# Optimization experiments

Measured on AMD Instinct MI355X. Metric: run time of the kernel, lower is better.

The kernel has to match this reference:

```python
import jax, jax.numpy as jnp
import numpy as np

N = 50000
E = 600000
F_IN = 256
H = 128            # num_hidden_units * num_heads (heads=1)
C = 20             # num_classes
NEG_SLOPE = 0.2    # PyG GATConv default


def setup_inputs() -> dict:
    key = jax.random.key(0)
    ks = jax.random.split(key, 16)
    g = lambda k, shape, fan: jax.random.normal(k, shape, jnp.float32) / np.sqrt(fan)
    return {
        "x": jax.random.normal(ks[0], (N, F_IN), jnp.float32),
        "edge_index": jax.random.randint(ks[1], (2, E), 0, N, jnp.int64),
        # GATConv 1: F_IN -> H (heads=1, concat)
        "W1": g(ks[2], (F_IN, H), F_IN),
        "a_src1": g(ks[3], (H,), H),
        "a_dst1": g(ks[4], (H,), H),
        "b1": jnp.zeros((H,), jnp.float32),
        # GATConv 2: H -> H (heads=1)
        "W2": g(ks[5], (H, H), H),
        "a_src2": g(ks[6], (H,), H),
        "a_dst2": g(ks[7], (H,), H),
        "b2": jnp.zeros((H,), jnp.float32),
        # MLP head
        "Wm1": g(ks[8], (H, H), H),
        "bm1": jnp.zeros((H,), jnp.float32),
        "Wm2": g(ks[9], (H, C), H),
        "bm2": jnp.zeros((C,), jnp.float32),
    }


def gat_layer(x, W, a_src, a_dst, b, src, dst, n_nodes):
    """Single-head GATConv (PyG semantics, self-loops already in src/dst)."""
    h = x @ W                                    # [N, H]
    # edge attention logits: leaky_relu(a_src . h_j + a_dst . h_i)
    logits = jax.nn.leaky_relu((h @ a_src)[src] + (h @ a_dst)[dst], NEG_SLOPE)  # [Etot]
    # softmax over incoming edges per target node
    m = jax.ops.segment_max(logits, dst, num_segments=n_nodes)
    e = jnp.exp(logits - m[dst])
    denom = jax.ops.segment_sum(e, dst, num_segments=n_nodes)
    coef = e / denom[dst]                        # [Etot]
    out = jax.ops.segment_sum(coef[:, None] * h[src], dst, num_segments=n_nodes)
    return out + b


def reference(x, edge_index, W1, a_src1, a_dst1, b1, W2, a_src2, a_dst2, b2, Wm1, bm1, Wm2, bm2):
    n = x.shape[0]
    loops = jnp.arange(n, dtype=edge_index.dtype)
    src = jnp.concatenate([edge_index[0], loops])  # add self loops (GATConv default)
    dst = jnp.concatenate([edge_index[1], loops])
    h = gat_layer(x, W1, a_src1, a_dst1, b1, src, dst, n)
    h = jax.nn.relu(h)                            # dropout = identity at eval
    h = gat_layer(h, W2, a_src2, a_dst2, b2, src, dst, n)
    # MLP head: Linear -> (dropout) -> ReLU -> Linear -> sigmoid
    z = jax.nn.relu(h @ Wm1 + bm1)
    return jax.nn.sigmoid(z @ Wm2 + bm2)
```

## Files before the change

kernel.cpp:

```cpp
#include <hip/hip_runtime.h>
#include <math.h>

#define F_IN 256
#define HDIM 128
#define NCLS 20
#define NEG_SLOPE 0.2f
#define SCAN_CHUNK 1024

typedef float f32x4 __attribute__((ext_vector_type(4)));
typedef _Float16 f16x2 __attribute__((ext_vector_type(2)));
typedef _Float16 f16x4 __attribute__((ext_vector_type(4)));
typedef _Float16 f16x8 __attribute__((ext_vector_type(8)));

static __device__ __forceinline__ float lrelu(float x) { return x > 0.f ? x : NEG_SLOPE * x; }

__global__ void count_kernel(const int* __restrict__ ei, int E, int N, int* __restrict__ deg) {
    int e = blockIdx.x * blockDim.x + threadIdx.x;
    int Etot = E + N;
    if (e >= Etot) return;
    int d = (e < E) ? ei[E + e] : (e - E);
    atomicAdd(&deg[d], 1);
}

__global__ __launch_bounds__(256) void scan_reduce_kernel(const int* __restrict__ deg, int n,
                                                          int* __restrict__ bsums) {
    int base = blockIdx.x * SCAN_CHUNK + threadIdx.x * 4;
    int s = 0;
    if (base + 3 < n) {
        int4 v = *reinterpret_cast<const int4*>(&deg[base]);
        s = v.x + v.y + v.z + v.w;
    } else {
#pragma unroll
        for (int j = 0; j < 4; ++j) if (base + j < n) s += deg[base + j];
    }
#pragma unroll
    for (int o = 32; o > 0; o >>= 1) s += __shfl_down(s, o);
    __shared__ int ws[4];
    int lane = threadIdx.x & 63, w = threadIdx.x >> 6;
    if (lane == 0) ws[w] = s;
    __syncthreads();
    if (threadIdx.x == 0) bsums[blockIdx.x] = ws[0] + ws[1] + ws[2] + ws[3];
}

__global__ __launch_bounds__(256) void scan_bsums_kernel(int* __restrict__ bsums, int nb,
                                                         int* __restrict__ off, int n) {
    __shared__ int sh[256];
    int tid = threadIdx.x;
    int v = (tid < nb) ? bsums[tid] : 0;
    sh[tid] = v;
    __syncthreads();
    for (int d = 1; d < 256; d <<= 1) {
        int t = (tid >= d) ? sh[tid - d] : 0;
        __syncthreads();
        sh[tid] += t;
        __syncthreads();
    }
    if (tid < nb) bsums[tid] = sh[tid] - v;
    if (tid == 255) off[n] = sh[255];
}

__global__ __launch_bounds__(256) void scan_down_kernel(const int* __restrict__ deg, int n,
                                                        const int* __restrict__ bpre,
                                                        int* __restrict__ off) {
    int base = blockIdx.x * SCAN_CHUNK + threadIdx.x * 4;
    int v0 = 0, v1 = 0, v2 = 0, v3 = 0;
    if (base + 3 < n) {
        int4 t = *reinterpret_cast<const int4*>(&deg[base]);
        v0 = t.x; v1 = t.y; v2 = t.z; v3 = t.w;
    } else {
        if (base + 0 < n) v0 = deg[base + 0];
        if (base + 1 < n) v1 = deg[base + 1];
        if (base + 2 < n) v2 = deg[base + 2];
        if (base + 3 < n) v3 = deg[base + 3];
    }
    int tsum = v0 + v1 + v2 + v3;
    int lane = threadIdx.x & 63, w = threadIdx.x >> 6;
    int inc = tsum;
#pragma unroll
    for (int o = 1; o < 64; o <<= 1) {
        int t = __shfl_up(inc, o);
        if (lane >= o) inc += t;
    }
    int texc = inc - tsum;
    __shared__ int wsum[4];
    if (lane == 63) wsum[w] = inc;
    __syncthreads();
    int wpre = 0;
    for (int i = 0; i < w; ++i) wpre += wsum[i];
    int p = bpre[blockIdx.x] + wpre + texc;
    if (base + 3 < n) {
        int4 o4;
        o4.x = p; o4.y = p + v0; o4.z = p + v0 + v1; o4.w = p + v0 + v1 + v2;
        *reinterpret_cast<int4*>(&off[base]) = o4;
    } else {
        int run = p;
        if (base + 0 < n) { off[base + 0] = run; run += v0; }
        if (base + 1 < n) { off[base + 1] = run; run += v1; }
        if (base + 2 < n) { off[base + 2] = run; run += v2; }
        if (base + 3 < n) { off[base + 3] = run; }
    }
}

__global__ void scatter_kernel(const int* __restrict__ ei, int E, int N,
                               const int* __restrict__ off, int* __restrict__ cursor,
                               int* __restrict__ csr_src) {
    int e = blockIdx.x * blockDim.x + threadIdx.x;
    int Etot = E + N;
    if (e >= Etot) return;
    int s, d;
    if (e < E) { s = ei[e]; d = ei[E + e]; } else { s = d = e - E; }
    int pos = off[d] + atomicAdd(&cursor[d], 1);
    csr_src[pos] = s;
}

__global__ __launch_bounds__(64) void pack_b_kernel(const float* __restrict__ W1,
                                                    const float* __restrict__ W2,
                                                    const float* __restrict__ Wm1,
                                                    _Float16* __restrict__ p1,
                                                    _Float16* __restrict__ p2,
                                                    _Float16* __restrict__ p3) {
    int t = blockIdx.x;
    int lane = threadIdx.x;
    const float* B; _Float16* out; int r;
    if (t < 64)      { B = W1;  out = p1; r = t; }
    else if (t < 96) { B = W2;  out = p2; r = t - 64; }
    else             { B = Wm1; out = p3; r = t - 96; }
    int ks = r >> 3, cf = r & 7;
    int c  = cf * 16 + (lane & 15);
    int k0 = ks * 32 + (lane >> 4) * 8;
    size_t base = ((size_t)r * 64 + lane) * 16;
#pragma unroll
    for (int i = 0; i < 8; ++i) {
        float v = B[(size_t)(k0 + i) * 128 + c];
        _Float16 h = (_Float16)v;
        out[base + i]     = h;
        out[base + 8 + i] = (_Float16)(v - (float)h);
    }
}

template <int AFMT, int KSTEPS, int FUSE_HEAD>
__global__ __launch_bounds__(512) void gemm_mfma_kernel(
        const void* __restrict__ Aptr, const _Float16* __restrict__ Bp,
        _Float16* __restrict__ C, int M,
        const float* __restrict__ bias, int act,
        const float* __restrict__ a_src, const float* __restrict__ a_dst,
        float* __restrict__ as_out, float* __restrict__ ad_out,
        const float* __restrict__ Wh, const float* __restrict__ bh2,
        float* __restrict__ outp) {
    constexpr int K = KSTEPS * 32;
    __shared__ float sal[2][4][64];
    __shared__ float zs[FUSE_HEAD ? 64 : 1][FUSE_HEAD ? 132 : 1];
    __shared__ float Wt[FUSE_HEAD ? 20 : 1][FUSE_HEAD ? 132 : 1];
    __shared__ float bb[FUSE_HEAD ? 20 : 1];

    int tid = threadIdx.x;
    int lane = tid & 63;
    int wid = tid >> 6;
    int wr = wid >> 2, wc = wid & 3;
    int bm = blockIdx.x * 64;
    int l15 = lane & 15, l4 = lane >> 4;
    int row0 = bm + wr * 32 + l15;
    int koff = l4 * 8;

    if constexpr (FUSE_HEAD) {
        for (int i = tid; i < HDIM * NCLS; i += 512) Wt[i % NCLS][i / NCLS] = Wh[i];
        if (tid < NCLS) bb[tid] = bh2[tid];
    }

    const float*    A32 = (const float*)Aptr;
    const _Float16* A16 = (const _Float16*)Aptr;
    bool ok0 = row0 < M, ok1 = (row0 + 16) < M;
    const f16x8 zf = {0, 0, 0, 0, 0, 0, 0, 0};

    f32x4 acc[2][2];
#pragma unroll
    for (int m = 0; m < 2; ++m)
#pragma unroll
        for (int j = 0; j < 2; ++j) acc[m][j] = (f32x4){0.f, 0.f, 0.f, 0.f};

    auto loadA = [&](int ks, f16x8 a[2]) {
        int kb = ks * 32 + koff;
#pragma unroll
        for (int m = 0; m < 2; ++m) {
            int rr = row0 + m * 16;
            bool ok = m ? ok1 : ok0;
            if (AFMT == 0) {
                if (ok) {
                    const float* p = &A32[(size_t)rr * K + kb];
                    float4 u = *reinterpret_cast<const float4*>(p);
                    float4 w = *reinterpret_cast<const float4*>(p + 4);
                    f16x8 t;
                    t[0] = (_Float16)u.x; t[1] = (_Float16)u.y;
                    t[2] = (_Float16)u.z; t[3] = (_Float16)u.w;
                    t[4] = (_Float16)w.x; t[5] = (_Float16)w.y;
                    t[6] = (_Float16)w.z; t[7] = (_Float16)w.w;
                    a[m] = t;
                } else a[m] = zf;
            } else {
                a[m] = ok ? *reinterpret_cast<const f16x8*>(&A16[(size_t)rr * K + kb]) : zf;
            }
        }
    };
    auto loadB = [&](int ks, f16x8 bh[2], f16x8 bl[2]) {
#pragma unroll
        for (int j = 0; j < 2; ++j) {
            int cf = wc * 2 + j;
            const _Float16* p = Bp + (((size_t)ks * 8 + cf) * 64 + lane) * 16;
            bh[j] = *reinterpret_cast<const f16x8*>(p);
            bl[j] = *reinterpret_cast<const f16x8*>(p + 8);
        }
    };

    f16x8 a0[2], a1[2], bh0[2], bh1[2], bl0[2], bl1[2];
    loadA(0, a0); loadB(0, bh0, bl0);
#pragma unroll
    for (int ks = 0; ks < KSTEPS; ks += 2) {
        loadA(ks + 1, a1); loadB(ks + 1, bh1, bl1);
#pragma unroll
        for (int j = 0; j < 2; ++j) {
            acc[0][j] = __builtin_amdgcn_mfma_f32_16x16x32_f16(a0[0], bh0[j], acc[0][j], 0, 0, 0);
            acc[1][j] = __builtin_amdgcn_mfma_f32_16x16x32_f16(a0[1], bh0[j], acc[1][j], 0, 0, 0);
            acc[0][j] = __builtin_amdgcn_mfma_f32_16x16x32_f16(a0[0], bl0[j], acc[0][j], 0, 0, 0);
            acc[1][j] = __builtin_amdgcn_mfma_f32_16x16x32_f16(a0[1], bl0[j], acc[1][j], 0, 0, 0);
        }
        if (ks + 2 < KSTEPS) { loadA(ks + 2, a0); loadB(ks + 2, bh0, bl0); }
#pragma unroll
        for (int j = 0; j < 2; ++j) {
            acc[0][j] = __builtin_amdgcn_mfma_f32_16x16x32_f16(a1[0], bh1[j], acc[0][j], 0, 0, 0);
            acc[1][j] = __builtin_amdgcn_mfma_f32_16x16x32_f16(a1[1], bh1[j], acc[1][j], 0, 0, 0);
            acc[0][j] = __builtin_amdgcn_mfma_f32_16x16x32_f16(a1[0], bl1[j], acc[0][j], 0, 0, 0);
            acc[1][j] = __builtin_amdgcn_mfma_f32_16x16x32_f16(a1[1], bl1[j], acc[1][j], 0, 0, 0);
        }
    }

    float ps[2][4], pd[2][4];
#pragma unroll
    for (int m = 0; m < 2; ++m)
#pragma unroll
        for (int reg = 0; reg < 4; ++reg) { ps[m][reg] = 0.f; pd[m][reg] = 0.f; }

#pragma unroll
    for (int j = 0; j < 2; ++j) {
        int col = wc * 32 + j * 16 + l15;
        float bi = bias ? bias[col] : 0.f;
        float asc = a_src ? a_src[col] : 0.f;
        float adc = a_src ? a_dst[col] : 0.f;
#pragma unroll
        for (int m = 0; m < 2; ++m) {
#pragma unroll
            for (int reg = 0; reg < 4; ++reg) {
                int rloc = wr * 32 + m * 16 + l4 * 4 + reg;
                int rr = bm + rloc;
                float v = acc[m][j][reg] + bi;
                if (act) v = fmaxf(v, 0.f);
                if constexpr (FUSE_HEAD) {
                    zs[rloc][col] = v;
                } else {
                    if (rr < M) C[(size_t)rr * 128 + col] = (_Float16)v;
                }
                ps[m][reg] = fmaf(v, asc, ps[m][reg]);
                pd[m][reg] = fmaf(v, adc, pd[m][reg]);
            }
        }
    }

    if (a_src) {
#pragma unroll
        for (int o = 1; o < 16; o <<= 1) {
#pragma unroll
            for (int m = 0; m < 2; ++m)
#pragma unroll
                for (int reg = 0; reg < 4; ++reg) {
                    ps[m][reg] += __shfl_xor(ps[m][reg], o);
                    pd[m][reg] += __shfl_xor(pd[m][reg], o);
                }
        }
        if (l15 == 0) {
#pragma unroll
            for (int m = 0; m < 2; ++m)
#pragma unroll
                for (int reg = 0; reg < 4; ++reg) {
                    int rloc = wr * 32 + m * 16 + l4 * 4 + reg;
                    sal[0][wc][rloc] = ps[m][reg];
                    sal[1][wc][rloc] = pd[m][reg];
                }
        }
        __syncthreads();
        if (tid < 64) {
            int rr = bm + tid;
            if (rr < M) {
                as_out[rr] = sal[0][0][tid] + sal[0][1][tid] + sal[0][2][tid] + sal[0][3][tid];
                ad_out[rr] = sal[1][0][tid] + sal[1][1][tid] + sal[1][2][tid] + sal[1][3][tid];
            }
        }
    }

    if constexpr (FUSE_HEAD) {
        __syncthreads();
        for (int idx = tid; idx < 64 * NCLS; idx += 512) {
            int r = idx / NCLS, c = idx % NCLS;
            int rr = bm + r;
            if (rr >= M) continue;
            float s = bb[c];
#pragma unroll
            for (int k = 0; k < HDIM; k += 4) {
                float4 z4 = *reinterpret_cast<const float4*>(&zs[r][k]);
                float4 w4 = *reinterpret_cast<const float4*>(&Wt[c][k]);
                s = fmaf(z4.x, w4.x, s);
                s = fmaf(z4.y, w4.y, s);
                s = fmaf(z4.z, w4.z, s);
                s = fmaf(z4.w, w4.w, s);
            }
            outp[(size_t)rr * NCLS + c] = 1.f / (1.f + __expf(-s));
        }
    }
}

__global__ __launch_bounds__(256) void aggregate_kernel(const _Float16* __restrict__ h,
                                 const float* __restrict__ asrc, const float* __restrict__ adst,
                                 const int* __restrict__ off, const int* __restrict__ csr_src,
                                 const float* __restrict__ bias,
                                 _Float16* __restrict__ out,
                                 int N, int do_relu) {
    __shared__ float2 sm[4][64];
    int wslot = threadIdx.x >> 6;
    int wave = blockIdx.x * 4 + wslot;
    int lane = threadIdx.x & 63;
    if (wave >= N) return;
    int o0 = off[wave], o1 = off[wave + 1];
    float ad = adst[wave];
    int l31 = lane & 31;
    int jst = lane >> 5;

    float denom = 0.f;
    float4 aA = make_float4(0.f, 0.f, 0.f, 0.f);
    float4 aB = make_float4(0.f, 0.f, 0.f, 0.f);

    for (int base = o0; base < o1; base += 64) {
        int cnt = o1 - base; if (cnt > 64) cnt = 64;
        float e = 0.f; int s = 0;
        if (lane < cnt) {
            s = csr_src[base + lane];
            e = __expf(lrelu(asrc[s] + ad));
        }
        float t = e;
#pragma unroll
        for (int o = 32; o > 0; o >>= 1) t += __shfl_xor(t, o);
        denom += t;
        sm[wslot][lane] = make_float2(__int_as_float(s), e);

        int j = jst;
        for (; j + 2 < cnt; j += 4) {
            float2 s0 = sm[wslot][j];
            float2 s1 = sm[wslot][j + 2];
            f16x4 h0 = *reinterpret_cast<const f16x4*>(&h[(size_t)__float_as_int(s0.x) * HDIM + 4 * l31]);
            f16x4 h1 = *reinterpret_cast<const f16x4*>(&h[(size_t)__float_as_int(s1.x) * HDIM + 4 * l31]);
            aA.x = fmaf(s0.y, (float)h0[0], aA.x);
            aA.y = fmaf(s0.y, (float)h0[1], aA.y);
            aA.z = fmaf(s0.y, (float)h0[2], aA.z);
            aA.w = fmaf(s0.y, (float)h0[3], aA.w);
            aB.x = fmaf(s1.y, (float)h1[0], aB.x);
            aB.y = fmaf(s1.y, (float)h1[1], aB.y);
            aB.z = fmaf(s1.y, (float)h1[2], aB.z);
            aB.w = fmaf(s1.y, (float)h1[3], aB.w);
        }
        if (j < cnt) {
            float2 s0 = sm[wslot][j];
            f16x4 h0 = *reinterpret_cast<const f16x4*>(&h[(size_t)__float_as_int(s0.x) * HDIM + 4 * l31]);
            aA.x = fmaf(s0.y, (float)h0[0], aA.x);
            aA.y = fmaf(s0.y, (float)h0[1], aA.y);
            aA.z = fmaf(s0.y, (float)h0[2], aA.z);
            aA.w = fmaf(s0.y, (float)h0[3], aA.w);
        }
    }

    aA.x += aB.x; aA.y += aB.y; aA.z += aB.z; aA.w += aB.w;
    aA.x += __shfl_xor(aA.x, 32);
    aA.y += __shfl_xor(aA.y, 32);
    aA.z += __shfl_xor(aA.z, 32);
    aA.w += __shfl_xor(aA.w, 32);

    if (lane < 32) {
        float inv = 1.f / denom;
        float4 bi = *reinterpret_cast<const float4*>(&bias[4 * l31]);
        float v0 = aA.x * inv + bi.x;
        float v1 = aA.y * inv + bi.y;
        float v2 = aA.z * inv + bi.z;
        float v3 = aA.w * inv + bi.w;
        if (do_relu) {
            v0 = fmaxf(v0, 0.f); v1 = fmaxf(v1, 0.f);
            v2 = fmaxf(v2, 0.f); v3 = fmaxf(v3, 0.f);
        }
        f16x4 o4;
        o4[0] = (_Float16)v0; o4[1] = (_Float16)v1;
        o4[2] = (_Float16)v2; o4[3] = (_Float16)v3;
        *reinterpret_cast<f16x4*>(&out[(size_t)wave * HDIM + 4 * l31]) = o4;
    }
}

extern "C" void kernel_launch(void* const* d_in, const int* in_sizes, int n_in,
                              void* d_out, int out_size, void* d_ws, size_t ws_size,
                              hipStream_t stream) {
    const float* x      = (const float*)d_in[0];
    const int*   ei     = (const int*)d_in[1];
    const float* W1     = (const float*)d_in[2];
    const float* a_src1 = (const float*)d_in[3];
    const float* a_dst1 = (const float*)d_in[4];
    const float* b1     = (const float*)d_in[5];
    const float* W2     = (const float*)d_in[6];
    const float* a_src2 = (const float*)d_in[7];
    const float* a_dst2 = (const float*)d_in[8];
    const float* b2     = (const float*)d_in[9];
    const float* Wm1    = (const float*)d_in[10];
    const float* bm1    = (const float*)d_in[11];
    const float* Wm2    = (const float*)d_in[12];
    const float* bm2    = (const float*)d_in[13];

    int N = in_sizes[0] / F_IN;
    int E = in_sizes[1] / 2;
    int Etot = E + N;

    char* ws = (char*)d_ws;
    size_t pos = 0;
    auto alloc = [&](size_t bytes) -> void* {
        void* p = ws + pos;
        pos = (pos + bytes + 255) & ~(size_t)255;
        return p;
    };
    _Float16* h16 = (_Float16*)alloc((size_t)N * HDIM * 2);
    _Float16* f16 = (_Float16*)alloc((size_t)N * HDIM * 2);
    float* as_buf = (float*)alloc((size_t)N * 4);
    float* ad_buf = (float*)alloc((size_t)N * 4);
    int*   deg    = (int*)alloc((size_t)N * 4);
    int*   offs   = (int*)alloc((size_t)(N + 1) * 4);
    int*   cursor = (int*)alloc((size_t)N * 4);
    int*   csr    = (int*)alloc((size_t)Etot * 4);
    int*   bsums  = (int*)alloc(256 * 4);
    _Float16* p1 = (_Float16*)alloc(65536 * 2);
    _Float16* p2 = (_Float16*)alloc(32768 * 2);
    _Float16* p3 = (_Float16*)alloc(32768 * 2);

    hipMemsetAsync(deg, 0, (size_t)N * 4, stream);
    hipMemsetAsync(cursor, 0, (size_t)N * 4, stream);

    int eb = (Etot + 255) / 256;
    int nb = (N + SCAN_CHUNK - 1) / SCAN_CHUNK;
    count_kernel<<<eb, 256, 0, stream>>>(ei, E, N, deg);
    scan_reduce_kernel<<<nb, 256, 0, stream>>>(deg, N, bsums);
    scan_bsums_kernel<<<1, 256, 0, stream>>>(bsums, nb, offs, N);
    scan_down_kernel<<<nb, 256, 0, stream>>>(deg, N, bsums, offs);
    scatter_kernel<<<eb, 256, 0, stream>>>(ei, E, N, offs, cursor, csr);

    pack_b_kernel<<<128, 64, 0, stream>>>(W1, W2, Wm1, p1, p2, p3);

    int gemm_blocks = (N + 63) / 64;
    int wave_blocks = (N + 3) / 4;

    gemm_mfma_kernel<0, 8, 0><<<gemm_blocks, 512, 0, stream>>>(x, p1, h16, N, nullptr, 0,
                                                               a_src1, a_dst1, as_buf, ad_buf,
                                                               nullptr, nullptr, nullptr);
    aggregate_kernel<<<wave_blocks, 256, 0, stream>>>(h16, as_buf, ad_buf, offs, csr, b1, f16, N, 1);

    gemm_mfma_kernel<1, 4, 0><<<gemm_blocks, 512, 0, stream>>>(f16, p2, h16, N, nullptr, 0,
                                                               a_src2, a_dst2, as_buf, ad_buf,
                                                               nullptr, nullptr, nullptr);
    aggregate_kernel<<<wave_blocks, 256, 0, stream>>>(h16, as_buf, ad_buf, offs, csr, b2, f16, N, 0);

    gemm_mfma_kernel<1, 4, 1><<<gemm_blocks, 512, 0, stream>>>(f16, p3, h16, N, bm1, 1,
                                                               nullptr, nullptr, nullptr, nullptr,
                                                               Wm2, bm2, (float*)d_out);
}
```

Measured before the change: 227.3 us.

## Widen GEMM wave tiles to 4 column fragments and gather 8 halves per lane

The GEMM now runs 4 waves of 256 threads, each computing 32 rows by 64 columns. Each A fragment is reused across four B fragments, which halves redundant A loads and the cross-wave logit reduction, at the cost of more accumulator and B registers per wave. The aggregation kernel now has each lane gather 16-byte f16x8 chunks, so four edges are processed per wave iteration instead of two. That widens each memory request and moves more edges in flight, but replaces the two interleaved accumulators with a single strided loop and adds a two-step shuffle reduction.

```diff
diff --git a/kernel.cpp b/kernel.cpp
--- a/kernel.cpp
+++ b/kernel.cpp
@@ -139,7 +139,7 @@
 }
 
 template <int AFMT, int KSTEPS, int FUSE_HEAD>
-__global__ __launch_bounds__(512) void gemm_mfma_kernel(
+__global__ __launch_bounds__(256) void gemm_mfma_kernel(
         const void* __restrict__ Aptr, const _Float16* __restrict__ Bp,
         _Float16* __restrict__ C, int M,
         const float* __restrict__ bias, int act,
@@ -148,7 +148,7 @@
         const float* __restrict__ Wh, const float* __restrict__ bh2,
         float* __restrict__ outp) {
     constexpr int K = KSTEPS * 32;
-    __shared__ float sal[2][4][64];
+    __shared__ float sal[2][2][64];
     __shared__ float zs[FUSE_HEAD ? 64 : 1][FUSE_HEAD ? 132 : 1];
     __shared__ float Wt[FUSE_HEAD ? 20 : 1][FUSE_HEAD ? 132 : 1];
     __shared__ float bb[FUSE_HEAD ? 20 : 1];
@@ -156,14 +156,14 @@
     int tid = threadIdx.x;
     int lane = tid & 63;
     int wid = tid >> 6;
-    int wr = wid >> 2, wc = wid & 3;
+    int wr = wid >> 1, wc = wid & 1;
     int bm = blockIdx.x * 64;
     int l15 = lane & 15, l4 = lane >> 4;
     int row0 = bm + wr * 32 + l15;
     int koff = l4 * 8;
 
     if constexpr (FUSE_HEAD) {
-        for (int i = tid; i < HDIM * NCLS; i += 512) Wt[i % NCLS][i / NCLS] = Wh[i];
+        for (int i = tid; i < HDIM * NCLS; i += 256) Wt[i % NCLS][i / NCLS] = Wh[i];
         if (tid < NCLS) bb[tid] = bh2[tid];
     }
 
@@ -172,11 +172,11 @@
     bool ok0 = row0 < M, ok1 = (row0 + 16) < M;
     const f16x8 zf = {0, 0, 0, 0, 0, 0, 0, 0};
 
-    f32x4 acc[2][2];
+    f32x4 acc[2][4];
 #pragma unroll
     for (int m = 0; m < 2; ++m)
 #pragma unroll
-        for (int j = 0; j < 2; ++j) acc[m][j] = (f32x4){0.f, 0.f, 0.f, 0.f};
+        for (int j = 0; j < 4; ++j) acc[m][j] = (f32x4){0.f, 0.f, 0.f, 0.f};
 
     auto loadA = [&](int ks, f16x8 a[2]) {
         int kb = ks * 32 + koff;
@@ -201,23 +201,23 @@
             }
         }
     };
-    auto loadB = [&](int ks, f16x8 bh[2], f16x8 bl[2]) {
-#pragma unroll
-        for (int j = 0; j < 2; ++j) {
-            int cf = wc * 2 + j;
+    auto loadB = [&](int ks, f16x8 bh[4], f16x8 bl[4]) {
+#pragma unroll
+        for (int j = 0; j < 4; ++j) {
+            int cf = wc * 4 + j;
             const _Float16* p = Bp + (((size_t)ks * 8 + cf) * 64 + lane) * 16;
             bh[j] = *reinterpret_cast<const f16x8*>(p);
             bl[j] = *reinterpret_cast<const f16x8*>(p + 8);
         }
     };
 
-    f16x8 a0[2], a1[2], bh0[2], bh1[2], bl0[2], bl1[2];
+    f16x8 a0[2], a1[2], bh0[4], bh1[4], bl0[4], bl1[4];
     loadA(0, a0); loadB(0, bh0, bl0);
 #pragma unroll
     for (int ks = 0; ks < KSTEPS; ks += 2) {
         loadA(ks + 1, a1); loadB(ks + 1, bh1, bl1);
 #pragma unroll
-        for (int j = 0; j < 2; ++j) {
+        for (int j = 0; j < 4; ++j) {
             acc[0][j] = __builtin_amdgcn_mfma_f32_16x16x32_f16(a0[0], bh0[j], acc[0][j], 0, 0, 0);
             acc[1][j] = __builtin_amdgcn_mfma_f32_16x16x32_f16(a0[1], bh0[j], acc[1][j], 0, 0, 0);
             acc[0][j] = __builtin_amdgcn_mfma_f32_16x16x32_f16(a0[0], bl0[j], acc[0][j], 0, 0, 0);
@@ -225,7 +225,7 @@
         }
         if (ks + 2 < KSTEPS) { loadA(ks + 2, a0); loadB(ks + 2, bh0, bl0); }
 #pragma unroll
-        for (int j = 0; j < 2; ++j) {
+        for (int j = 0; j < 4; ++j) {
             acc[0][j] = __builtin_amdgcn_mfma_f32_16x16x32_f16(a1[0], bh1[j], acc[0][j], 0, 0, 0);
             acc[1][j] = __builtin_amdgcn_mfma_f32_16x16x32_f16(a1[1], bh1[j], acc[1][j], 0, 0, 0);
             acc[0][j] = __builtin_amdgcn_mfma_f32_16x16x32_f16(a1[0], bl1[j], acc[0][j], 0, 0, 0);
@@ -240,8 +240,8 @@
         for (int reg = 0; reg < 4; ++reg) { ps[m][reg] = 0.f; pd[m][reg] = 0.f; }
 
 #pragma unroll
-    for (int j = 0; j < 2; ++j) {
-        int col = wc * 32 + j * 16 + l15;
+    for (int j = 0; j < 4; ++j) {
+        int col = wc * 64 + j * 16 + l15;
         float bi = bias ? bias[col] : 0.f;
         float asc = a_src ? a_src[col] : 0.f;
         float adc = a_src ? a_dst[col] : 0.f;
@@ -289,15 +289,15 @@
         if (tid < 64) {
             int rr = bm + tid;
             if (rr < M) {
-                as_out[rr] = sal[0][0][tid] + sal[0][1][tid] + sal[0][2][tid] + sal[0][3][tid];
-                ad_out[rr] = sal[1][0][tid] + sal[1][1][tid] + sal[1][2][tid] + sal[1][3][tid];
+                as_out[rr] = sal[0][0][tid] + sal[0][1][tid];
+                ad_out[rr] = sal[1][0][tid] + sal[1][1][tid];
             }
         }
     }
 
     if constexpr (FUSE_HEAD) {
         __syncthreads();
-        for (int idx = tid; idx < 64 * NCLS; idx += 512) {
+        for (int idx = tid; idx < 64 * NCLS; idx += 256) {
             int r = idx / NCLS, c = idx % NCLS;
             int rr = bm + r;
             if (rr >= M) continue;
@@ -329,12 +329,13 @@
     if (wave >= N) return;
     int o0 = off[wave], o1 = off[wave + 1];
     float ad = adst[wave];
-    int l31 = lane & 31;
-    int jst = lane >> 5;
+    int l15 = lane & 15;
+    int eslot = lane >> 4;
 
     float denom = 0.f;
-    float4 aA = make_float4(0.f, 0.f, 0.f, 0.f);
-    float4 aB = make_float4(0.f, 0.f, 0.f, 0.f);
+    float acc[8];
+#pragma unroll
+    for (int i = 0; i < 8; ++i) acc[i] = 0.f;
 
     for (int base = o0; base < o1; base += 64) {
         int cnt = o1 - base; if (cnt > 64) cnt = 64;
@@ -348,53 +349,34 @@
         for (int o = 32; o > 0; o >>= 1) t += __shfl_xor(t, o);
         denom += t;
         sm[wslot][lane] = make_float2(__int_as_float(s), e);
-
-        int j = jst;
-        for (; j + 2 < cnt; j += 4) {
-            float2 s0 = sm[wslot][j];
-            float2 s1 = sm[wslot][j + 2];
-            f16x4 h0 = *reinterpret_cast<const f16x4*>(&h[(size_t)__float_as_int(s0.x) * HDIM + 4 * l31]);
-            f16x4 h1 = *reinterpret_cast<const f16x4*>(&h[(size_t)__float_as_int(s1.x) * HDIM + 4 * l31]);
-            aA.x = fmaf(s0.y, (float)h0[0], aA.x);
-            aA.y = fmaf(s0.y, (float)h0[1], aA.y);
-            aA.z = fmaf(s0.y, (float)h0[2], aA.z);
-            aA.w = fmaf(s0.y, (float)h0[3], aA.w);
-            aB.x = fmaf(s1.y, (float)h1[0], aB.x);
-            aB.y = fmaf(s1.y, (float)h1[1], aB.y);
-            aB.z = fmaf(s1.y, (float)h1[2], aB.z);
-            aB.w = fmaf(s1.y, (float)h1[3], aB.w);
-        }
-        if (j < cnt) {
-            float2 s0 = sm[wslot][j];
-            f16x4 h0 = *reinterpret_cast<const f16x4*>(&h[(size_t)__float_as_int(s0.x) * HDIM + 4 * l31]);
-            aA.x = fmaf(s0.y, (float)h0[0], aA.x);
-            aA.y = fmaf(s0.y, (float)h0[1], aA.y);
-            aA.z = fmaf(s0.y, (float)h0[2], aA.z);
-            aA.w = fmaf(s0.y, (float)h0[3], aA.w);
-        }
-    }
-
-    aA.x += aB.x; aA.y += aB.y; aA.z += aB.z; aA.w += aB.w;
-    aA.x += __shfl_xor(aA.x, 32);
-    aA.y += __shfl_xor(aA.y, 32);
-    aA.z += __shfl_xor(aA.z, 32);
-    aA.w += __shfl_xor(aA.w, 32);
-
-    if (lane < 32) {
+        for (int j = eslot; j < cnt; j += 4) {
+            float2 se = sm[wslot][j];
+            int s0 = __float_as_int(se.x);
+            f16x8 hv = *reinterpret_cast<const f16x8*>(&h[(size_t)s0 * HDIM + 8 * l15]);
+#pragma unroll
+            for (int i = 0; i < 8; ++i) acc[i] = fmaf(se.y, (float)hv[i], acc[i]);
+        }
+    }
+
+#pragma unroll
+    for (int i = 0; i < 8; ++i) {
+        acc[i] += __shfl_xor(acc[i], 16);
+        acc[i] += __shfl_xor(acc[i], 32);
+    }
+
+    if (lane < 16) {
         float inv = 1.f / denom;
-        float4 bi = *reinterpret_cast<const float4*>(&bias[4 * l31]);
-        float v0 = aA.x * inv + bi.x;
-        float v1 = aA.y * inv + bi.y;
-        float v2 = aA.z * inv + bi.z;
-        float v3 = aA.w * inv + bi.w;
-        if (do_relu) {
-            v0 = fmaxf(v0, 0.f); v1 = fmaxf(v1, 0.f);
-            v2 = fmaxf(v2, 0.f); v3 = fmaxf(v3, 0.f);
-        }
-        f16x4 o4;
-        o4[0] = (_Float16)v0; o4[1] = (_Float16)v1;
-        o4[2] = (_Float16)v2; o4[3] = (_Float16)v3;
-        *reinterpret_cast<f16x4*>(&out[(size_t)wave * HDIM + 4 * l31]) = o4;
+        float4 b0 = *reinterpret_cast<const float4*>(&bias[8 * l15]);
+        float4 b1 = *reinterpret_cast<const float4*>(&bias[8 * l15 + 4]);
+        float bv[8] = {b0.x, b0.y, b0.z, b0.w, b1.x, b1.y, b1.z, b1.w};
+        f16x8 o8;
+#pragma unroll
+        for (int i = 0; i < 8; ++i) {
+            float v = acc[i] * inv + bv[i];
+            if (do_relu) v = fmaxf(v, 0.f);
+            o8[i] = (_Float16)v;
+        }
+        *reinterpret_cast<f16x8*>(&out[(size_t)wave * HDIM + 8 * l15]) = o8;
     }
 }
 
@@ -456,17 +438,17 @@
     int gemm_blocks = (N + 63) / 64;
     int wave_blocks = (N + 3) / 4;
 
-    gemm_mfma_kernel<0, 8, 0><<<gemm_blocks, 512, 0, stream>>>(x, p1, h16, N, nullptr, 0,
+    gemm_mfma_kernel<0, 8, 0><<<gemm_blocks, 256, 0, stream>>>(x, p1, h16, N, nullptr, 0,
                                                                a_src1, a_dst1, as_buf, ad_buf,
                                                                nullptr, nullptr, nullptr);
     aggregate_kernel<<<wave_blocks, 256, 0, stream>>>(h16, as_buf, ad_buf, offs, csr, b1, f16, N, 1);
 
-    gemm_mfma_kernel<1, 4, 0><<<gemm_blocks, 512, 0, stream>>>(f16, p2, h16, N, nullptr, 0,
+    gemm_mfma_kernel<1, 4, 0><<<gemm_blocks, 256, 0, stream>>>(f16, p2, h16, N, nullptr, 0,
                                                                a_src2, a_dst2, as_buf, ad_buf,
                                                                nullptr, nullptr, nullptr);
     aggregate_kernel<<<wave_blocks, 256, 0, stream>>>(h16, as_buf, ad_buf, offs, csr, b2, f16, N, 0);
 
-    gemm_mfma_kernel<1, 4, 1><<<gemm_blocks, 512, 0, stream>>>(f16, p3, h16, N, bm1, 1,
+    gemm_mfma_kernel<1, 4, 1><<<gemm_blocks, 256, 0, stream>>>(f16, p3, h16, N, bm1, 1,
                                                                nullptr, nullptr, nullptr, nullptr,
                                                                Wm2, bm2, (float*)d_out);
 }
```

Result: faster. 213.1 us, median of 3 (-6.2%).
